# Kernel optimization log

Hardware: AMD Instinct MI355X
Metric: run time of the kernel (lower is better)

The kernel has to match this reference:

```python
import jax, jax.numpy as jnp
import numpy as np

NFFT = 512
HOP = 256
N_FREQ = NFFT // 2


def _imdct_kernels():
    # Matches _get_imdct_kernels: windowed IMDCT cosine basis, shape [nfft, nfft//2]
    def kernel_fn(time, freq):
        win = np.sin(np.pi * (2 * time + 1) / (2.0 * NFFT))
        return np.cos(np.pi / NFFT * (2 * time + 1 + NFFT / 2.0) * (freq + 0.5)) * win
    k = np.fromfunction(kernel_fn, (NFFT, N_FREQ), dtype=np.float64)
    return jnp.asarray(k.astype(np.float32))  # [nfft, n_freq]


def setup_inputs() -> dict:
    key = jax.random.key(0)
    spec = jax.random.normal(key, (16, 1, N_FREQ, 4096), dtype=jnp.float32)
    return {"spec": spec, "kernels": _imdct_kernels()}


def reference(spec, kernels):
    # spec: [B, 1, n_freq, T]; kernels: [nfft, n_freq]
    B, _, _, T = spec.shape
    # conv2d with (n_freq,1) kernel == per-frame basis matmul over frequency
    frames = jnp.einsum('bft,kf->btk', spec[:, 0], kernels) * (4.0 / NFFT)  # [B, T, nfft]
    # conv_transpose2d with identity-diagonal kernel and stride=hop == overlap-add
    L = (T - 1) * HOP + NFFT
    idx = jnp.arange(T)[:, None] * HOP + jnp.arange(NFFT)[None, :]  # [T, nfft]
    out = jnp.zeros((B, L), dtype=spec.dtype).at[:, idx].add(frames)
    return out
```

## Files before the change

kernel.cpp:

```cpp
#include <hip/hip_runtime.h>
#include <stdint.h>

#define NFREQ 256
#define NB 16
#define NT 4096
#define LOUT 1048832
#define TROWS 65
#define TROW 132

typedef __bf16 bf16;
typedef __bf16 bf16x8 __attribute__((ext_vector_type(8)));
typedef float floatx4 __attribute__((ext_vector_type(4)));

__device__ inline uint32_t f_as_u(float x) { union { float f; uint32_t u; } v; v.f = x; return v.u; }
__device__ inline uint32_t bf16r(float x) {
    uint32_t u = f_as_u(x);
    return (u + 0x7fffu + ((u >> 16) & 1u)) >> 16;
}

__global__ __launch_bounds__(256) void build_kb(const float* __restrict__ ker,
                                                bf16* __restrict__ kbF) {
    int idx = blockIdx.x * 256 + threadIdx.x;
    int n = idx >> 9, f = idx & 511;
    float v = (f < 256) ? ker[(n + 256) * 256 + f] : ker[n * 256 + (f - 256)];
    uint32_t rr = bf16r(v * 0.0078125f);
    union { uint16_t u; bf16 b; } o; o.u = (uint16_t)rr;
    kbF[((size_t)(f >> 5) * 256 + n) * 32 + (f & 31)] = o.b;
}

__global__ __launch_bounds__(256, 4) void imdct_gemm(const float* __restrict__ spec,
                                                     const bf16* __restrict__ kbF,
                                                     float* __restrict__ out) {
    __shared__ uint32_t Tt[TROWS * TROW];

    const int jt = blockIdx.x;
    const int b  = blockIdx.y;
    const int tid = threadIdx.x, lane = tid & 63, w = tid >> 6;
    const int j0 = jt * 64;
    const float* sb = spec + (size_t)b * NFREQ * NT;

    {
        const int lpar = lane & 1, lt = lane >> 1;
        const int fpw = w * 32;
        #pragma unroll 1
        for (int rb = 0; rb < 4; ++rb) {
            const int tc = rb >> 1;
            const int fh = (rb & 1) * 16;
            const int t  = j0 - 1 + tc * 32 + lt;
            const bool tok = ((unsigned)t < (unsigned)NT);
            const float* pb = sb + (size_t)((fpw + fh) * 2 + lpar) * NT + t;
            float v[16];
            #pragma unroll
            for (int i = 0; i < 16; ++i)
                v[i] = tok ? pb[(size_t)i * 2 * NT] : 0.0f;
            const int tl = tc * 32 + lt;
            uint32_t* dst = &Tt[tl * TROW + fpw + fh];
            #pragma unroll
            for (int i = 0; i < 16; i += 4) {
                uint32_t pk[4];
                #pragma unroll
                for (int u = 0; u < 4; ++u) {
                    uint32_t h = bf16r(v[i + u]);
                    uint32_t o = (uint32_t)__shfl_xor((int)h, 1);
                    pk[u] = (h & 0xffffu) | (o << 16);
                }
                if (lpar == 0) {
                    uint4 q4; q4.x = pk[0]; q4.y = pk[1]; q4.z = pk[2]; q4.w = pk[3];
                    *reinterpret_cast<uint4*>(dst + i) = q4;
                }
            }
        }
        {
            int f = w * 64 + lane;
            int te = j0 + 63;
            float v = ((unsigned)te < (unsigned)NT) ? sb[(size_t)f * NT + te] : 0.0f;
            uint32_t h = bf16r(v); uint32_t o = (uint32_t)__shfl_xor((int)h, 1);
            if (lpar == 0) Tt[64 * TROW + w * 32 + lt] = (h & 0xffffu) | (o << 16);
        }
    }
    __syncthreads();

    const int row16 = lane & 15, q = lane >> 4;
    floatx4 acc[4][4] = {};
    const uint8_t* Tb = reinterpret_cast<const uint8_t*>(Tt);
    const bf16* kbw = kbF + (size_t)w * 64 * 32 + (row16 * 32 + q * 8);

    #pragma unroll 1
    for (int kki = 0; kki < 8; ++kki) {
        const int toff = kki >> 2;
        const int kbyte = (kki & 3) * 128;
        const uint8_t* ta = Tb + (size_t)(row16 + toff) * 528 + kbyte + q * 16;
        const bf16* kb2 = kbw + (size_t)kki * 16384;
        #pragma unroll
        for (int ks = 0; ks < 2; ++ks) {
            bf16x8 af[4], bfr[4];
            #pragma unroll
            for (int jn = 0; jn < 4; ++jn)
                bfr[jn] = *reinterpret_cast<const bf16x8*>(
                    kb2 + (size_t)ks * 8192 + jn * 512);
            #pragma unroll
            for (int i = 0; i < 4; ++i)
                af[i] = *reinterpret_cast<const bf16x8*>(ta + ks * 64 + i * 8448);
            #pragma unroll
            for (int i = 0; i < 4; ++i)
                #pragma unroll
                for (int jn = 0; jn < 4; ++jn)
                    acc[i][jn] = __builtin_amdgcn_mfma_f32_16x16x32_bf16(af[i], bfr[jn], acc[i][jn], 0, 0, 0);
        }
    }

    #pragma unroll
    for (int i = 0; i < 4; ++i) {
        #pragma unroll
        for (int e = 0; e < 4; ++e) {
            int j = j0 + i * 16 + q * 4 + e;
            if (j <= 4096) {
                float* orow = out + (size_t)b * LOUT + (size_t)j * 256 + w * 64;
                #pragma unroll
                for (int jn = 0; jn < 4; ++jn)
                    orow[jn * 16 + row16] = acc[i][jn][e];
            }
        }
    }
}

extern "C" void kernel_launch(void* const* d_in, const int* in_sizes, int n_in,
                              void* d_out, int out_size, void* d_ws, size_t ws_size,
                              hipStream_t stream) {
    const float* spec = (const float*)d_in[0];
    const float* ker  = (const float*)d_in[1];
    float* out = (float*)d_out;

    bf16* kbF = (bf16*)d_ws;

    build_kb<<<512, 256, 0, stream>>>(ker, kbF);
    imdct_gemm<<<dim3(65, NB), 256, 0, stream>>>(spec, kbF, out);
}
```

Measured before the change: 140.2 us.

## Pre-transpose spectrum to swizzled bf16 buffer and stream it into LDS directly

Adds a separate pass that converts the spectrum to bf16, transposes it to time-major rows, and XOR-swizzles the columns into a workspace buffer. The GEMM kernel then fills shared memory with direct global-to-LDS loads and reads fragments through the swizzle. The aim is to drop the strided fp32 loads, shuffles and packing from the GEMM prologue and to avoid LDS bank conflicts. In exchange it adds an extra kernel and a full write and re-read of the spectrum in bf16, and the fast path only runs when the workspace is large enough.

```diff
diff --git a/kernel.cpp b/kernel.cpp
--- a/kernel.cpp
+++ b/kernel.cpp
@@ -7,6 +7,10 @@
 #define LOUT 1048832
 #define TROWS 65
 #define TROW 132
+#define SROWS 4224
+#define ROW0 8
+#define KB_BYTES 262144
+#define WS_NEED (KB_BYTES + (size_t)NB * SROWS * 512)
 
 typedef __bf16 bf16;
 typedef __bf16 bf16x8 __attribute__((ext_vector_type(8)));
@@ -28,17 +32,113 @@
     kbF[((size_t)(f >> 5) * 256 + n) * 32 + (f & 31)] = o.b;
 }
 
+__global__ __launch_bounds__(256) void build_specT(const float* __restrict__ spec,
+                                                   uint16_t* __restrict__ sT) {
+    __shared__ __align__(16) uint16_t S[64 * 260];
+    const int b  = blockIdx.y;
+    const int t0 = blockIdx.x * 64 - ROW0;
+    const int tid = threadIdx.x;
+    const int tx = tid & 63, ty = tid >> 6;
+    const float* sb = spec + (size_t)b * NFREQ * NT;
+    const int t = t0 + tx;
+    const bool tok = ((unsigned)t < (unsigned)NT);
+    #pragma unroll 4
+    for (int fq = 0; fq < 64; ++fq) {
+        int f = fq * 4 + ty;
+        float v = tok ? sb[(size_t)f * NT + t] : 0.0f;
+        S[tx * 260 + f] = (uint16_t)bf16r(v);
+    }
+    __syncthreads();
+    const int w = tid >> 6, lane = tid & 63;
+    #pragma unroll 1
+    for (int rr = 0; rr < 16; ++rr) {
+        int r = w * 16 + rr;
+        int tg = t0 + r;
+        int k = (tg + 1) & 7;
+        uint2 v = *reinterpret_cast<const uint2*>(&S[r * 260 + lane * 4]);
+        uint16_t* drow = sT + ((size_t)b * SROWS + (tg + ROW0)) * 256;
+        int dst = (((lane >> 1) ^ k) << 3) + ((lane & 1) << 2);
+        *reinterpret_cast<uint2*>(&drow[dst]) = v;
+    }
+}
+
+__global__ __launch_bounds__(256, 4) void imdct_gemm_f(const uint16_t* __restrict__ sT,
+                                                       const bf16* __restrict__ kbF,
+                                                       float* __restrict__ out) {
+    __shared__ __align__(16) uint16_t T[66 * 256];
+    const int jt = blockIdx.x, b = blockIdx.y;
+    const int tid = threadIdx.x, lane = tid & 63, w = tid >> 6;
+    const int j0 = jt * 64;
+    const char* sB = (const char*)(sT + ((size_t)b * SROWS + (size_t)(j0 - 1 + ROW0)) * 256);
+
+    {
+        const char* gp0 = sB + lane * 16;
+        #pragma unroll 1
+        for (int r2 = w; r2 < 33; r2 += 4) {
+            __builtin_amdgcn_global_load_lds(
+                (const __attribute__((address_space(1))) uint32_t*)(gp0 + r2 * 1024),
+                (__attribute__((address_space(3))) uint32_t*)((char*)T + r2 * 1024),
+                16, 0, 0);
+        }
+        asm volatile("s_waitcnt vmcnt(0)" ::: "memory");
+    }
+    __syncthreads();
+
+    const int row16 = lane & 15, q = lane >> 4;
+    floatx4 acc[4][4] = {};
+    const char* Tb = (const char*)T;
+    const bf16* kbw = kbF + (size_t)w * 64 * 32 + (row16 * 32 + q * 8);
+    const int swz0 = (row16 & 7) << 4, swz1 = ((row16 + 1) & 7) << 4;
+
+    #pragma unroll 1
+    for (int kki = 0; kki < 8; ++kki) {
+        const int toff = kki >> 2;
+        const int kbyte = (kki & 3) * 128;
+        const char* ta = Tb + (size_t)(row16 + toff) * 512;
+        const int sz = toff ? swz1 : swz0;
+        const bf16* kb2 = kbw + (size_t)kki * 16384;
+        #pragma unroll
+        for (int ks = 0; ks < 2; ++ks) {
+            bf16x8 af[4], bfr[4];
+            #pragma unroll
+            for (int jn = 0; jn < 4; ++jn)
+                bfr[jn] = *reinterpret_cast<const bf16x8*>(kb2 + (size_t)ks * 8192 + jn * 512);
+            const int col = (kbyte + ks * 64 + q * 16) ^ sz;
+            #pragma unroll
+            for (int i = 0; i < 4; ++i)
+                af[i] = *reinterpret_cast<const bf16x8*>(ta + i * 8192 + col);
+            #pragma unroll
+            for (int i = 0; i < 4; ++i)
+                #pragma unroll
+                for (int jn = 0; jn < 4; ++jn)
+                    acc[i][jn] = __builtin_amdgcn_mfma_f32_16x16x32_bf16(af[i], bfr[jn], acc[i][jn], 0, 0, 0);
+        }
+    }
+
+    #pragma unroll
+    for (int i = 0; i < 4; ++i) {
+        #pragma unroll
+        for (int e = 0; e < 4; ++e) {
+            int j = j0 + i * 16 + q * 4 + e;
+            if (j <= 4096) {
+                float* orow = out + (size_t)b * LOUT + (size_t)j * 256 + w * 64;
+                #pragma unroll
+                for (int jn = 0; jn < 4; ++jn)
+                    orow[jn * 16 + row16] = acc[i][jn][e];
+            }
+        }
+    }
+}
+
 __global__ __launch_bounds__(256, 4) void imdct_gemm(const float* __restrict__ spec,
                                                      const bf16* __restrict__ kbF,
                                                      float* __restrict__ out) {
     __shared__ uint32_t Tt[TROWS * TROW];
-
     const int jt = blockIdx.x;
     const int b  = blockIdx.y;
     const int tid = threadIdx.x, lane = tid & 63, w = tid >> 6;
     const int j0 = jt * 64;
     const float* sb = spec + (size_t)b * NFREQ * NT;
-
     {
         const int lpar = lane & 1, lt = lane >> 1;
         const int fpw = w * 32;
@@ -79,12 +179,10 @@
         }
     }
     __syncthreads();
-
     const int row16 = lane & 15, q = lane >> 4;
     floatx4 acc[4][4] = {};
     const uint8_t* Tb = reinterpret_cast<const uint8_t*>(Tt);
     const bf16* kbw = kbF + (size_t)w * 64 * 32 + (row16 * 32 + q * 8);
-
     #pragma unroll 1
     for (int kki = 0; kki < 8; ++kki) {
         const int toff = kki >> 2;
@@ -96,8 +194,7 @@
             bf16x8 af[4], bfr[4];
             #pragma unroll
             for (int jn = 0; jn < 4; ++jn)
-                bfr[jn] = *reinterpret_cast<const bf16x8*>(
-                    kb2 + (size_t)ks * 8192 + jn * 512);
+                bfr[jn] = *reinterpret_cast<const bf16x8*>(kb2 + (size_t)ks * 8192 + jn * 512);
             #pragma unroll
             for (int i = 0; i < 4; ++i)
                 af[i] = *reinterpret_cast<const bf16x8*>(ta + ks * 64 + i * 8448);
@@ -108,7 +205,6 @@
                     acc[i][jn] = __builtin_amdgcn_mfma_f32_16x16x32_bf16(af[i], bfr[jn], acc[i][jn], 0, 0, 0);
         }
     }
-
     #pragma unroll
     for (int i = 0; i < 4; ++i) {
         #pragma unroll
@@ -132,7 +228,13 @@
     float* out = (float*)d_out;
 
     bf16* kbF = (bf16*)d_ws;
-
     build_kb<<<512, 256, 0, stream>>>(ker, kbF);
-    imdct_gemm<<<dim3(65, NB), 256, 0, stream>>>(spec, kbF, out);
-}
+
+    if (ws_size >= WS_NEED) {
+        uint16_t* sTt = (uint16_t*)((char*)d_ws + KB_BYTES);
+        build_specT<<<dim3(66, NB), 256, 0, stream>>>(spec, sTt);
+        imdct_gemm_f<<<dim3(65, NB), 256, 0, stream>>>(sTt, kbF, out);
+    } else {
+        imdct_gemm<<<dim3(65, NB), 256, 0, stream>>>(spec, kbF, out);
+    }
+}
```

After: 184.0 us. +31.3%, slower.
